# Kernel optimization log

Hardware: AMD Instinct MI355X
Metric: run time of the kernel (lower is better)

Reference implementation:

```python
import jax, jax.numpy as jnp
import numpy as np

N_HEAD = 16
D_K = 64
D_V = 64
D_MODEL = 1024
B = 2
S = 2048
LN_EPS = 1e-6
NEG = -1000000000.0


def setup_inputs() -> dict:
    key = jax.random.key(0)
    ks = jax.random.split(key, 6)
    scale = 1.0 / np.sqrt(D_MODEL)
    return {
        "qkv": jax.random.normal(ks[0], (B, S, D_MODEL), dtype=jnp.float32),
        "mask": jax.random.randint(ks[1], (B, S, S), 0, 2, dtype=jnp.int32),
        "w_qs": jax.random.normal(ks[2], (D_MODEL, N_HEAD * D_K), dtype=jnp.float32) * scale,
        "w_ks": jax.random.normal(ks[3], (D_MODEL, N_HEAD * D_K), dtype=jnp.float32) * scale,
        "w_vs": jax.random.normal(ks[4], (D_MODEL, N_HEAD * D_V), dtype=jnp.float32) * scale,
        "w_fc": jax.random.normal(ks[5], (N_HEAD * D_V, D_MODEL), dtype=jnp.float32) * scale,
        "ln_gamma": jnp.ones((D_MODEL,), dtype=jnp.float32),
        "ln_beta": jnp.zeros((D_MODEL,), dtype=jnp.float32),
    }


def reference(qkv, mask, w_qs, w_ks, w_vs, w_fc, ln_gamma, ln_beta):
    b, s, d = qkv.shape
    temperature = jnp.asarray(D_K, qkv.dtype) ** 0.5
    residual = qkv
    # projections -> [b, h, s, d_k/d_v]
    q = (qkv @ w_qs).reshape(b, s, N_HEAD, D_K).transpose(0, 2, 1, 3)
    k = (qkv @ w_ks).reshape(b, s, N_HEAD, D_K).transpose(0, 2, 1, 3)
    v = (qkv @ w_vs).reshape(b, s, N_HEAD, D_V).transpose(0, 2, 1, 3)
    # scaled dot-product attention with mask
    attn = jnp.einsum('bhqd,bhkd->bhqk', q / temperature, k)
    attn = jnp.where(mask[:, None, :, :] == 0, jnp.asarray(NEG, attn.dtype), attn)
    attn = jax.nn.softmax(attn, axis=-1)
    out = jnp.einsum('bhqk,bhkd->bhqd', attn, v)
    # merge heads, output projection, residual + layernorm
    out = out.transpose(0, 2, 1, 3).reshape(b, s, N_HEAD * D_V)
    out = out @ w_fc
    out = out + residual
    mu = jnp.mean(out, axis=-1, keepdims=True)
    var = jnp.var(out, axis=-1, keepdims=True)
    out = (out - mu) * jax.lax.rsqrt(var + LN_EPS) * ln_gamma + ln_beta
    return out, attn
```

## Files before the change

### kernel.cpp

```cpp
#include <hip/hip_runtime.h>
#include <stdint.h>

#define D_MODEL 1024
#define NHEAD   16
#define BATCH   2
#define SEQ     2048
#define MROWS   (BATCH*SEQ)
#define OUT0_ELEMS (MROWS*D_MODEL)
#define W_ELEMS    (D_MODEL*D_MODEL)

#define U_QKV_HI  0
#define U_QKV_LO  4194304
#define U_WQ_HI   8388608
#define U_WQ_LO   9437184
#define U_WK_HI   10485760
#define U_WK_LO   11534336
#define U_WV      12582912
#define U_WFC     13631488
#define F_Q       7340032
#define F_K       11534336
#define U_VT      31457280
#define B_MB      71303168
#define F_G       2097152

typedef __bf16  bf16x8 __attribute__((ext_vector_type(8)));
typedef float   f32x4  __attribute__((ext_vector_type(4)));

__device__ __forceinline__ float bf2f(unsigned short u) {
    union { unsigned int ui; float f; } v; v.ui = ((unsigned int)u) << 16; return v.f;
}
__device__ __forceinline__ unsigned short f2bf(float f) {
    union { float f; unsigned int u; } v; v.f = f;
    unsigned int u = v.u;
    return (unsigned short)((u + 0x7FFFu + ((u >> 16) & 1u)) >> 16);
}
__device__ __forceinline__ void split2(float x, unsigned short& hi, unsigned short& lo) {
    hi = f2bf(x);
    lo = f2bf(x - bf2f(hi));
}

__global__ void k_split(const float* in, unsigned short* hiA, unsigned short* loA)
{
    int i = (blockIdx.x * 256 + threadIdx.x) * 4;
    float4 x = *(const float4*)&in[i];
    ushort4 h, l;
    split2(x.x, h.x, l.x); split2(x.y, h.y, l.y);
    split2(x.z, h.z, l.z); split2(x.w, h.w, l.w);
    *(ushort4*)&hiA[i] = h;
    *(ushort4*)&loA[i] = l;
}

__global__ void k_wtrans(const float* w0, const float* w1, const float* w2,
                         const float* w3, unsigned short* R)
{
    __shared__ __align__(16) float T[64][68];
    int z = blockIdx.z;
    const float* in = (z == 0) ? w0 : (z == 1) ? w1 : (z == 2) ? w2 : w3;
    const int hiOff[4] = {U_WQ_HI, U_WK_HI, U_WV, U_WFC};
    const int loOff[2] = {U_WQ_LO, U_WK_LO};
    unsigned short* outH = R + hiOff[z];
    unsigned short* outL = (z < 2) ? (R + loOff[z]) : nullptr;
    int bn = blockIdx.x, bk = blockIdx.y, tid = threadIdx.x;
    int r0 = tid >> 4, c = (tid & 15) * 4;
    for (int i = 0; i < 4; i++) {
        int r = r0 + i * 16;
        *(float4*)&T[r][c] = *(const float4*)&in[(bk*64 + r)*1024 + bn*64 + c];
    }
    __syncthreads();
    for (int i = 0; i < 4; i++) {
        int r = r0 + i * 16;
        ushort4 h, l;
        split2(T[c+0][r], h.x, l.x); split2(T[c+1][r], h.y, l.y);
        split2(T[c+2][r], h.z, l.z); split2(T[c+3][r], h.w, l.w);
        *(ushort4*)&outH[(bn*64 + r)*1024 + bk*64 + c] = h;
        if (z < 2) *(ushort4*)&outL[(bn*64 + r)*1024 + bk*64 + c] = l;
    }
}

__global__ void k_maskpack(const int* mask, unsigned long long* mb)
{
    int w = blockIdx.x * 4 + (threadIdx.x >> 6);
    int lane = threadIdx.x & 63;
    int v = mask[(size_t)w * 64 + lane];
    unsigned long long bal = __ballot(v != 0);
    if (lane == 0) mb[w] = bal;
}

__global__ __launch_bounds__(256)
void k_gemm_qk(const unsigned short* R, float* ws_f)
{
    __shared__ __align__(16) unsigned short Ah[8192], Al[8192];
    __shared__ __align__(16) unsigned short Bh[8192], Bl[8192];
    int tid = threadIdx.x, wv = tid >> 6, lane = tid & 63;
    int quad = lane >> 4, l15 = lane & 15;
    int m0 = blockIdx.y * 128, n0 = blockIdx.x * 128;
    int z = blockIdx.z;
    const unsigned short* Ahg = R + U_QKV_HI;
    const unsigned short* Alg = R + U_QKV_LO;
    const unsigned short* Bhg = R + (z == 0 ? U_WQ_HI : U_WK_HI);
    const unsigned short* Blg = R + (z == 0 ? U_WQ_LO : U_WK_LO);
    float* out = ws_f + (z == 0 ? F_Q : F_K);
    float scale = (z == 0) ? 0.125f : 1.0f;

    f32x4 zero4 = {0.f, 0.f, 0.f, 0.f};
    f32x4 acc[4][4];
    for (int a = 0; a < 4; a++) for (int b = 0; b < 4; b++) acc[a][b] = zero4;
    int wr = (wv >> 1) * 64, wc = (wv & 1) * 64;

    for (int k0 = 0; k0 < 1024; k0 += 64) {
        __syncthreads();
        for (int i = 0; i < 4; i++) {
            int e = (tid + 256*i) * 8, row = e >> 6, col = e & 63;
            *(uint4*)&Ah[e] = *(const uint4*)&Ahg[(m0+row)*1024 + k0 + col];
            *(uint4*)&Al[e] = *(const uint4*)&Alg[(m0+row)*1024 + k0 + col];
            *(uint4*)&Bh[e] = *(const uint4*)&Bhg[(n0+row)*1024 + k0 + col];
            *(uint4*)&Bl[e] = *(const uint4*)&Blg[(n0+row)*1024 + k0 + col];
        }
        __syncthreads();
        #pragma unroll
        for (int kc = 0; kc < 2; kc++) {
            bf16x8 ah[4], al[4], bh[4], bl[4];
            #pragma unroll
            for (int t = 0; t < 4; t++) {
                int ao = (wr + t*16 + l15)*64 + kc*32 + quad*8;
                int bo = (wc + t*16 + l15)*64 + kc*32 + quad*8;
                ah[t] = *(const bf16x8*)&Ah[ao];
                al[t] = *(const bf16x8*)&Al[ao];
                bh[t] = *(const bf16x8*)&Bh[bo];
                bl[t] = *(const bf16x8*)&Bl[bo];
            }
            #pragma unroll
            for (int tm = 0; tm < 4; tm++)
                #pragma unroll
                for (int tn = 0; tn < 4; tn++) {
                    acc[tm][tn] = __builtin_amdgcn_mfma_f32_16x16x32_bf16(ah[tm], bh[tn], acc[tm][tn], 0,0,0);
                    acc[tm][tn] = __builtin_amdgcn_mfma_f32_16x16x32_bf16(ah[tm], bl[tn], acc[tm][tn], 0,0,0);
                    acc[tm][tn] = __builtin_amdgcn_mfma_f32_16x16x32_bf16(al[tm], bh[tn], acc[tm][tn], 0,0,0);
                }
        }
    }
    for (int tm = 0; tm < 4; tm++) for (int tn = 0; tn < 4; tn++)
        for (int r = 0; r < 4; r++) {
            int row = m0 + wr + tm*16 + quad*4 + r;
            int col = n0 + wc + tn*16 + l15;
            out[(size_t)row*1024 + col] = acc[tm][tn][r] * scale;
        }
}

__global__ __launch_bounds__(256)
void k_gemm_bf(const unsigned short* A, const unsigned short* Bt,
               unsigned short* Vt, float* Gf, const float* resf, int mode)
{
    __shared__ __align__(16) unsigned short As[8192];
    __shared__ __align__(16) unsigned short Bs[8192];
    int tid = threadIdx.x, wv = tid >> 6, lane = tid & 63;
    int quad = lane >> 4, l15 = lane & 15;
    int m0 = blockIdx.y * 128, n0 = blockIdx.x * 128;
    f32x4 zero4 = {0.f, 0.f, 0.f, 0.f};
    f32x4 acc[4][4];
    for (int a = 0; a < 4; a++) for (int b = 0; b < 4; b++) acc[a][b] = zero4;
    int wr = (wv >> 1) * 64, wc = (wv & 1) * 64;

    for (int k0 = 0; k0 < 1024; k0 += 64) {
        __syncthreads();
        for (int i = 0; i < 4; i++) {
            int e = (tid + 256*i) * 8, row = e >> 6, col = e & 63;
            *(uint4*)&As[e] = *(const uint4*)&A [(m0+row)*1024 + k0 + col];
            *(uint4*)&Bs[e] = *(const uint4*)&Bt[(n0+row)*1024 + k0 + col];
        }
        __syncthreads();
        #pragma unroll
        for (int kc = 0; kc < 2; kc++) {
            bf16x8 af[4], bfr[4];
            #pragma unroll
            for (int t = 0; t < 4; t++) {
                af[t]  = *(const bf16x8*)&As[(wr + t*16 + l15)*64 + kc*32 + quad*8];
                bfr[t] = *(const bf16x8*)&Bs[(wc + t*16 + l15)*64 + kc*32 + quad*8];
            }
            #pragma unroll
            for (int tm = 0; tm < 4; tm++)
                #pragma unroll
                for (int tn = 0; tn < 4; tn++)
                    acc[tm][tn] = __builtin_amdgcn_mfma_f32_16x16x32_bf16(
                        af[tm], bfr[tn], acc[tm][tn], 0, 0, 0);
        }
    }
    for (int tm = 0; tm < 4; tm++) for (int tn = 0; tn < 4; tn++)
        for (int r = 0; r < 4; r++) {
            int row = m0 + wr + tm*16 + quad*4 + r;
            int col = n0 + wc + tn*16 + l15;
            float v = acc[tm][tn][r];
            if (mode == 1) {
                Gf[(size_t)row*1024 + col] = v + resf[(size_t)row*1024 + col];
            } else {
                int b = row >> 11, s = row & 2047, h = col >> 6, d = col & 63;
                Vt[(size_t)(((b*16 + h)*64 + d))*2048 + s] = f2bf(v);
            }
        }
}

__global__ __launch_bounds__(256)
void k_attn(const float* Q, const float* K, const unsigned short* Vt,
            const unsigned long long* mb, float* Pout, unsigned short* Obuf)
{
    __shared__ __align__(16) unsigned short Qh[128*64], Ql[128*64];
    __shared__ __align__(16) unsigned short Kh[32*64],  Kl[32*64];
    __shared__ __align__(16) unsigned short Vs[64*32];
    __shared__ __align__(16) unsigned short Ps[128*32];
    int tid = threadIdx.x, wv = tid >> 6, lane = tid & 63;
    int quad = lane >> 4, l15 = lane & 15;
    int h = blockIdx.x, qt = blockIdx.y, b = blockIdx.z;

    const float* Qb = Q + (size_t)(b*2048 + qt*128)*1024 + h*64;
    const float* Kb = K + (size_t)b*2048*1024 + h*64;
    const unsigned short* Vtb = Vt + (size_t)((b*16 + h)*64)*2048;
    const unsigned long long* Mb = mb + (size_t)(b*2048 + qt*128)*32;
    float* Pg = Pout + (size_t)((b*16 + h)*2048 + qt*128)*2048;

    for (int i = 0; i < 8; i++) {
        int e = (tid + 256*i)*4, row = e >> 6, col = e & 63;
        float4 x = *(const float4*)&Qb[(size_t)row*1024 + col];
        ushort4 hv, lv;
        split2(x.x, hv.x, lv.x); split2(x.y, hv.y, lv.y);
        split2(x.z, hv.z, lv.z); split2(x.w, hv.w, lv.w);
        *(ushort4*)&Qh[row*64 + col] = hv;
        *(ushort4*)&Ql[row*64 + col] = lv;
    }

    float lsum[8];
    for (int r = 0; r < 8; r++) lsum[r] = 0.f;
    f32x4 zero4 = {0.f, 0.f, 0.f, 0.f};

    for (int kt = 0; kt < 64; kt++) {
        __syncthreads();
        for (int i = 0; i < 2; i++) {
            int e = (tid + 256*i)*4, row = e >> 6, col = e & 63;
            float4 x = *(const float4*)&Kb[(size_t)(kt*32 + row)*1024 + col];
            ushort4 hv, lv;
            split2(x.x, hv.x, lv.x); split2(x.y, hv.y, lv.y);
            split2(x.z, hv.z, lv.z); split2(x.w, hv.w, lv.w);
            *(ushort4*)&Kh[row*64 + col] = hv;
            *(ushort4*)&Kl[row*64 + col] = lv;
        }
        __syncthreads();
        f32x4 sacc[2][2];
        for (int a = 0; a < 2; a++) for (int c = 0; c < 2; c++) sacc[a][c] = zero4;
        #pragma unroll
        for (int kc = 0; kc < 2; kc++) {
            bf16x8 qh[2], ql[2], kh[2], kl[2];
            #pragma unroll
            for (int t = 0; t < 2; t++) {
                int qo = (wv*32 + t*16 + l15)*64 + kc*32 + quad*8;
                int ko = (t*16 + l15)*64 + kc*32 + quad*8;
                qh[t] = *(const bf16x8*)&Qh[qo]; ql[t] = *(const bf16x8*)&Ql[qo];
                kh[t] = *(const bf16x8*)&Kh[ko]; kl[t] = *(const bf16x8*)&Kl[ko];
            }
            #pragma unroll
            for (int tm = 0; tm < 2; tm++)
                #pragma unroll
                for (int tn = 0; tn < 2; tn++) {
                    sacc[tm][tn] = __builtin_amdgcn_mfma_f32_16x16x32_bf16(qh[tm], kh[tn], sacc[tm][tn], 0,0,0);
                    sacc[tm][tn] = __builtin_amdgcn_mfma_f32_16x16x32_bf16(qh[tm], kl[tn], sacc[tm][tn], 0,0,0);
                    sacc[tm][tn] = __builtin_amdgcn_mfma_f32_16x16x32_bf16(ql[tm], kh[tn], sacc[tm][tn], 0,0,0);
                }
        }
        #pragma unroll
        for (int tm = 0; tm < 2; tm++)
            #pragma unroll
            for (int r = 0; r < 4; r++) {
                int row = wv*32 + tm*16 + quad*4 + r;
                unsigned long long w = Mb[row*32 + (kt >> 1)];
                int base = (kt & 1) * 32;
                float acc = 0.f;
                #pragma unroll
                for (int tn = 0; tn < 2; tn++)
                    if ((w >> (base + tn*16 + l15)) & 1ull) acc += __expf(sacc[tm][tn][r]);
                lsum[tm*4 + r] += acc;
            }
    }
    float invl[8];
    for (int r = 0; r < 8; r++) {
        float v = lsum[r];
        v += __shfl_xor(v, 1); v += __shfl_xor(v, 2);
        v += __shfl_xor(v, 4); v += __shfl_xor(v, 8);
        invl[r] = 1.0f / fmaxf(v, 1e-30f);
    }

    f32x4 oacc[2][4];
    for (int a = 0; a < 2; a++) for (int c = 0; c < 4; c++) oacc[a][c] = zero4;

    for (int kt = 0; kt < 64; kt++) {
        __syncthreads();
        for (int i = 0; i < 2; i++) {
            int e = (tid + 256*i)*4, row = e >> 6, col = e & 63;
            float4 x = *(const float4*)&Kb[(size_t)(kt*32 + row)*1024 + col];
            ushort4 hv, lv;
            split2(x.x, hv.x, lv.x); split2(x.y, hv.y, lv.y);
            split2(x.z, hv.z, lv.z); split2(x.w, hv.w, lv.w);
            *(ushort4*)&Kh[row*64 + col] = hv;
            *(ushort4*)&Kl[row*64 + col] = lv;
        }
        {
            int d = tid >> 2, sl = (tid & 3) * 8;
            *(uint4*)&Vs[d*32 + sl] = *(const uint4*)&Vtb[(size_t)d*2048 + kt*32 + sl];
        }
        __syncthreads();
        f32x4 sacc[2][2];
        for (int a = 0; a < 2; a++) for (int c = 0; c < 2; c++) sacc[a][c] = zero4;
        #pragma unroll
        for (int kc = 0; kc < 2; kc++) {
            bf16x8 qh[2], ql[2], kh[2], kl[2];
            #pragma unroll
            for (int t = 0; t < 2; t++) {
                int qo = (wv*32 + t*16 + l15)*64 + kc*32 + quad*8;
                int ko = (t*16 + l15)*64 + kc*32 + quad*8;
                qh[t] = *(const bf16x8*)&Qh[qo]; ql[t] = *(const bf16x8*)&Ql[qo];
                kh[t] = *(const bf16x8*)&Kh[ko]; kl[t] = *(const bf16x8*)&Kl[ko];
            }
            #pragma unroll
            for (int tm = 0; tm < 2; tm++)
                #pragma unroll
                for (int tn = 0; tn < 2; tn++) {
                    sacc[tm][tn] = __builtin_amdgcn_mfma_f32_16x16x32_bf16(qh[tm], kh[tn], sacc[tm][tn], 0,0,0);
                    sacc[tm][tn] = __builtin_amdgcn_mfma_f32_16x16x32_bf16(qh[tm], kl[tn], sacc[tm][tn], 0,0,0);
                    sacc[tm][tn] = __builtin_amdgcn_mfma_f32_16x16x32_bf16(ql[tm], kh[tn], sacc[tm][tn], 0,0,0);
                }
        }
        #pragma unroll
        for (int tm = 0; tm < 2; tm++)
            #pragma unroll
            for (int r = 0; r < 4; r++) {
                int row = wv*32 + tm*16 + quad*4 + r;
                unsigned long long w = Mb[row*32 + (kt >> 1)];
                int base = (kt & 1) * 32;
                float il = invl[tm*4 + r];
                #pragma unroll
                for (int tn = 0; tn < 2; tn++) {
                    float p = ((w >> (base + tn*16 + l15)) & 1ull)
                              ? __expf(sacc[tm][tn][r]) * il : 0.0f;
                    Ps[row*32 + tn*16 + l15] = f2bf(p);
                    Pg[(size_t)row*2048 + kt*32 + tn*16 + l15] = p;
                }
            }
        __syncthreads();
        {
            bf16x8 ap[2], bv[4];
            #pragma unroll
            for (int t = 0; t < 2; t++)
                ap[t] = *(const bf16x8*)&Ps[(wv*32 + t*16 + l15)*32 + quad*8];
            #pragma unroll
            for (int t = 0; t < 4; t++)
                bv[t] = *(const bf16x8*)&Vs[(t*16 + l15)*32 + quad*8];
            #pragma unroll
            for (int tm = 0; tm < 2; tm++)
                #pragma unroll
                for (int nd = 0; nd < 4; nd++)
                    oacc[tm][nd] = __builtin_amdgcn_mfma_f32_16x16x32_bf16(
                        ap[tm], bv[nd], oacc[tm][nd], 0, 0, 0);
        }
    }
    for (int tm = 0; tm < 2; tm++) for (int nd = 0; nd < 4; nd++)
        for (int r = 0; r < 4; r++) {
            int row = wv*32 + tm*16 + quad*4 + r;
            int grow = b*2048 + qt*128 + row;
            Obuf[(size_t)grow*1024 + h*64 + nd*16 + l15] = f2bf(oacc[tm][nd][r]);
        }
}

__global__ void k_ln(const float* G, const float* gamma, const float* beta,
                     float* out)
{
    int r = blockIdx.x, tid = threadIdx.x;
    float4 x = *(const float4*)&G[(size_t)r*1024 + tid*4];
    float s  = x.x + x.y + x.z + x.w;
    float sq = x.x*x.x + x.y*x.y + x.z*x.z + x.w*x.w;
    for (int d = 1; d < 64; d <<= 1) { s += __shfl_xor(s, d); sq += __shfl_xor(sq, d); }
    __shared__ float ssum[4], ssq[4];
    int wv = tid >> 6, lane = tid & 63;
    if (lane == 0) { ssum[wv] = s; ssq[wv] = sq; }
    __syncthreads();
    float ts = ssum[0] + ssum[1] + ssum[2] + ssum[3];
    float tq = ssq[0] + ssq[1] + ssq[2] + ssq[3];
    float mu  = ts * (1.0f/1024.0f);
    float var = tq * (1.0f/1024.0f) - mu*mu;
    float rs  = rsqrtf(var + 1e-6f);
    float4 o;
    int c = tid*4;
    o.x = (x.x - mu) * rs * gamma[c+0] + beta[c+0];
    o.y = (x.y - mu) * rs * gamma[c+1] + beta[c+1];
    o.z = (x.z - mu) * rs * gamma[c+2] + beta[c+2];
    o.w = (x.w - mu) * rs * gamma[c+3] + beta[c+3];
    *(float4*)&out[(size_t)r*1024 + c] = o;
}

extern "C" void kernel_launch(void* const* d_in, const int* in_sizes, int n_in,
                              void* d_out, int out_size, void* d_ws, size_t ws_size,
                              hipStream_t stream)
{
    const float* qkv   = (const float*)d_in[0];
    const int*   mask  = (const int*)d_in[1];
    const float* wq    = (const float*)d_in[2];
    const float* wk    = (const float*)d_in[3];
    const float* wvp   = (const float*)d_in[4];
    const float* wfc   = (const float*)d_in[5];
    const float* gamma = (const float*)d_in[6];
    const float* beta  = (const float*)d_in[7];

    unsigned short* R   = (unsigned short*)d_ws;
    float*          Wf  = (float*)d_ws;
    unsigned short* Vtb = R + U_VT;
    unsigned short* Ob  = R + U_QKV_HI;
    float*          Gf  = Wf + F_G;
    unsigned long long* MB = (unsigned long long*)((char*)d_ws + B_MB);

    float* outp  = (float*)d_out;
    float* attnp = outp + OUT0_ELEMS;

    k_split   <<<4096, 256, 0, stream>>>(qkv, R + U_QKV_HI, R + U_QKV_LO);
    k_wtrans  <<<dim3(16,16,4), 256, 0, stream>>>(wq, wk, wvp, wfc, R);
    k_maskpack<<<32768, 256, 0, stream>>>(mask, MB);
    k_gemm_qk <<<dim3(8,32,2), 256, 0, stream>>>(R, Wf);
    k_gemm_bf <<<dim3(8,32,1), 256, 0, stream>>>(R + U_QKV_HI, R + U_WV,
                                                 Vtb, nullptr, nullptr, 0);
    k_attn    <<<dim3(16,16,2), 256, 0, stream>>>(Wf + F_Q, Wf + F_K, Vtb, MB,
                                                  attnp, Ob);
    k_gemm_bf <<<dim3(8,32,1), 256, 0, stream>>>(Ob, R + U_WFC,
                                                 nullptr, Gf, qkv, 1);
    k_ln      <<<4096, 256, 0, stream>>>(Gf, gamma, beta, outp);
}
```

Measured before the change: 1.074 ms.

## Pre-split Q/K to bf16 hi/lo head-major, use LDS direct loads, widen attention key tiles

The Q/K projection GEMM now writes bf16 hi/lo splits in a head-major [b,h,s,d] layout instead of fp32. The attention kernel can then load Q, K and V tiles with global_load_lds directly, with no per-tile fp32 split. Key tiles grow from 32 to 64 columns, which halves loop iterations and removes one barrier per PV step, and the P staging buffer gets a padded stride. The GEMM kernels also switch to direct-to-LDS loads. The workspace layout is reshuffled, and reusing the old weight region for V^T relies on stage ordering being correct.

```diff
diff --git a/kernel.cpp b/kernel.cpp
--- a/kernel.cpp
+++ b/kernel.cpp
@@ -9,19 +9,22 @@
 #define OUT0_ELEMS (MROWS*D_MODEL)
 #define W_ELEMS    (D_MODEL*D_MODEL)
 
-#define U_QKV_HI  0
-#define U_QKV_LO  4194304
-#define U_WQ_HI   8388608
-#define U_WQ_LO   9437184
-#define U_WK_HI   10485760
-#define U_WK_LO   11534336
-#define U_WV      12582912
-#define U_WFC     13631488
-#define F_Q       7340032
-#define F_K       11534336
-#define U_VT      31457280
-#define B_MB      71303168
-#define F_G       2097152
+#define U_QKVH 0
+#define U_QKVL 4194304
+#define U_WQH  8388608
+#define U_WQL  9437184
+#define U_WKH  10485760
+#define U_WKL  11534336
+#define U_WV   12582912
+#define U_WFC  13631488
+#define U_QH   14680064
+#define U_QL   18874368
+#define U_KH   23068672
+#define U_KL   27262976
+#define U_VT   8388608
+#define U_MB   31457280
+#define F_G    2097152
+#define PS_LD  80
 
 typedef __bf16  bf16x8 __attribute__((ext_vector_type(8)));
 typedef float   f32x4  __attribute__((ext_vector_type(4)));
@@ -37,6 +40,11 @@
 __device__ __forceinline__ void split2(float x, unsigned short& hi, unsigned short& lo) {
     hi = f2bf(x);
     lo = f2bf(x - bf2f(hi));
+}
+__device__ __forceinline__ void gld16(const void* g, void* l) {
+    __builtin_amdgcn_global_load_lds(
+        (const __attribute__((address_space(1))) unsigned int*)g,
+        (__attribute__((address_space(3))) unsigned int*)l, 16, 0, 0);
 }
 
 __global__ void k_split(const float* in, unsigned short* hiA, unsigned short* loA)
@@ -56,8 +64,8 @@
     __shared__ __align__(16) float T[64][68];
     int z = blockIdx.z;
     const float* in = (z == 0) ? w0 : (z == 1) ? w1 : (z == 2) ? w2 : w3;
-    const int hiOff[4] = {U_WQ_HI, U_WK_HI, U_WV, U_WFC};
-    const int loOff[2] = {U_WQ_LO, U_WK_LO};
+    const int hiOff[4] = {U_WQH, U_WKH, U_WV, U_WFC};
+    const int loOff[2] = {U_WQL, U_WKL};
     unsigned short* outH = R + hiOff[z];
     unsigned short* outL = (z < 2) ? (R + loOff[z]) : nullptr;
     int bn = blockIdx.x, bk = blockIdx.y, tid = threadIdx.x;
@@ -87,7 +95,7 @@
 }
 
 __global__ __launch_bounds__(256)
-void k_gemm_qk(const unsigned short* R, float* ws_f)
+void k_gemm_qk(const unsigned short* R, unsigned short* RW)
 {
     __shared__ __align__(16) unsigned short Ah[8192], Al[8192];
     __shared__ __align__(16) unsigned short Bh[8192], Bl[8192];
@@ -95,11 +103,12 @@
     int quad = lane >> 4, l15 = lane & 15;
     int m0 = blockIdx.y * 128, n0 = blockIdx.x * 128;
     int z = blockIdx.z;
-    const unsigned short* Ahg = R + U_QKV_HI;
-    const unsigned short* Alg = R + U_QKV_LO;
-    const unsigned short* Bhg = R + (z == 0 ? U_WQ_HI : U_WK_HI);
-    const unsigned short* Blg = R + (z == 0 ? U_WQ_LO : U_WK_LO);
-    float* out = ws_f + (z == 0 ? F_Q : F_K);
+    const unsigned short* Ahg = R + U_QKVH;
+    const unsigned short* Alg = R + U_QKVL;
+    const unsigned short* Bhg = R + (z == 0 ? U_WQH : U_WKH);
+    const unsigned short* Blg = R + (z == 0 ? U_WQL : U_WKL);
+    unsigned short* outH = RW + (z == 0 ? U_QH : U_KH);
+    unsigned short* outL = RW + (z == 0 ? U_QL : U_KL);
     float scale = (z == 0) ? 0.125f : 1.0f;
 
     f32x4 zero4 = {0.f, 0.f, 0.f, 0.f};
@@ -111,10 +120,10 @@
         __syncthreads();
         for (int i = 0; i < 4; i++) {
             int e = (tid + 256*i) * 8, row = e >> 6, col = e & 63;
-            *(uint4*)&Ah[e] = *(const uint4*)&Ahg[(m0+row)*1024 + k0 + col];
-            *(uint4*)&Al[e] = *(const uint4*)&Alg[(m0+row)*1024 + k0 + col];
-            *(uint4*)&Bh[e] = *(const uint4*)&Bhg[(n0+row)*1024 + k0 + col];
-            *(uint4*)&Bl[e] = *(const uint4*)&Blg[(n0+row)*1024 + k0 + col];
+            gld16(&Ahg[(m0+row)*1024 + k0 + col], &Ah[e]);
+            gld16(&Alg[(m0+row)*1024 + k0 + col], &Al[e]);
+            gld16(&Bhg[(n0+row)*1024 + k0 + col], &Bh[e]);
+            gld16(&Blg[(n0+row)*1024 + k0 + col], &Bl[e]);
         }
         __syncthreads();
         #pragma unroll
@@ -143,7 +152,12 @@
         for (int r = 0; r < 4; r++) {
             int row = m0 + wr + tm*16 + quad*4 + r;
             int col = n0 + wc + tn*16 + l15;
-            out[(size_t)row*1024 + col] = acc[tm][tn][r] * scale;
+            int bb = row >> 11, s = row & 2047, hh = col >> 6, d = col & 63;
+            size_t idx = ((size_t)(bb*16 + hh)*2048 + s)*64 + d;
+            unsigned short hv, lv;
+            split2(acc[tm][tn][r] * scale, hv, lv);
+            outH[idx] = hv;
+            outL[idx] = lv;
         }
 }
 
@@ -165,8 +179,8 @@
         __syncthreads();
         for (int i = 0; i < 4; i++) {
             int e = (tid + 256*i) * 8, row = e >> 6, col = e & 63;
-            *(uint4*)&As[e] = *(const uint4*)&A [(m0+row)*1024 + k0 + col];
-            *(uint4*)&Bs[e] = *(const uint4*)&Bt[(n0+row)*1024 + k0 + col];
+            gld16(&A [(m0+row)*1024 + k0 + col], &As[e]);
+            gld16(&Bt[(n0+row)*1024 + k0 + col], &Bs[e]);
         }
         __syncthreads();
         #pragma unroll
@@ -200,65 +214,63 @@
 }
 
 __global__ __launch_bounds__(256)
-void k_attn(const float* Q, const float* K, const unsigned short* Vt,
-            const unsigned long long* mb, float* Pout, unsigned short* Obuf)
+void k_attn(const unsigned short* R, const unsigned long long* mb,
+            float* Pout, unsigned short* Obuf)
 {
     __shared__ __align__(16) unsigned short Qh[128*64], Ql[128*64];
-    __shared__ __align__(16) unsigned short Kh[32*64],  Kl[32*64];
-    __shared__ __align__(16) unsigned short Vs[64*32];
-    __shared__ __align__(16) unsigned short Ps[128*32];
+    __shared__ __align__(16) unsigned short Kh[64*64],  Kl[64*64];
+    __shared__ __align__(16) unsigned short Vs[64*64];
+    __shared__ __align__(16) unsigned short Ps[128*PS_LD];
     int tid = threadIdx.x, wv = tid >> 6, lane = tid & 63;
     int quad = lane >> 4, l15 = lane & 15;
     int h = blockIdx.x, qt = blockIdx.y, b = blockIdx.z;
-
-    const float* Qb = Q + (size_t)(b*2048 + qt*128)*1024 + h*64;
-    const float* Kb = K + (size_t)b*2048*1024 + h*64;
-    const unsigned short* Vtb = Vt + (size_t)((b*16 + h)*64)*2048;
+    int bh = b*16 + h;
+
+    const unsigned short* Qhg = R + U_QH + ((size_t)bh*2048 + qt*128)*64;
+    const unsigned short* Qlg = R + U_QL + ((size_t)bh*2048 + qt*128)*64;
+    const unsigned short* Khg = R + U_KH + (size_t)bh*2048*64;
+    const unsigned short* Klg = R + U_KL + (size_t)bh*2048*64;
+    const unsigned short* Vtg = R + U_VT + (size_t)bh*64*2048;
     const unsigned long long* Mb = mb + (size_t)(b*2048 + qt*128)*32;
-    float* Pg = Pout + (size_t)((b*16 + h)*2048 + qt*128)*2048;
-
-    for (int i = 0; i < 8; i++) {
-        int e = (tid + 256*i)*4, row = e >> 6, col = e & 63;
-        float4 x = *(const float4*)&Qb[(size_t)row*1024 + col];
-        ushort4 hv, lv;
-        split2(x.x, hv.x, lv.x); split2(x.y, hv.y, lv.y);
-        split2(x.z, hv.z, lv.z); split2(x.w, hv.w, lv.w);
-        *(ushort4*)&Qh[row*64 + col] = hv;
-        *(ushort4*)&Ql[row*64 + col] = lv;
+    float* Pg = Pout + ((size_t)bh*2048 + qt*128)*2048;
+
+    for (int i = 0; i < 4; i++) {
+        int e = (tid + 256*i)*8;
+        gld16(&Qhg[e], &Qh[e]);
+        gld16(&Qlg[e], &Ql[e]);
     }
 
     float lsum[8];
     for (int r = 0; r < 8; r++) lsum[r] = 0.f;
     f32x4 zero4 = {0.f, 0.f, 0.f, 0.f};
 
-    for (int kt = 0; kt < 64; kt++) {
+    for (int kt = 0; kt < 32; kt++) {
         __syncthreads();
         for (int i = 0; i < 2; i++) {
-            int e = (tid + 256*i)*4, row = e >> 6, col = e & 63;
-            float4 x = *(const float4*)&Kb[(size_t)(kt*32 + row)*1024 + col];
-            ushort4 hv, lv;
-            split2(x.x, hv.x, lv.x); split2(x.y, hv.y, lv.y);
-            split2(x.z, hv.z, lv.z); split2(x.w, hv.w, lv.w);
-            *(ushort4*)&Kh[row*64 + col] = hv;
-            *(ushort4*)&Kl[row*64 + col] = lv;
-        }
-        __syncthreads();
-        f32x4 sacc[2][2];
-        for (int a = 0; a < 2; a++) for (int c = 0; c < 2; c++) sacc[a][c] = zero4;
+            int e = (tid + 256*i)*8;
+            gld16(&Khg[kt*4096 + e], &Kh[e]);
+            gld16(&Klg[kt*4096 + e], &Kl[e]);
+        }
+        __syncthreads();
+        f32x4 sacc[2][4];
+        for (int a = 0; a < 2; a++) for (int c = 0; c < 4; c++) sacc[a][c] = zero4;
         #pragma unroll
         for (int kc = 0; kc < 2; kc++) {
-            bf16x8 qh[2], ql[2], kh[2], kl[2];
+            bf16x8 qh[2], ql[2], kh[4], kl[4];
             #pragma unroll
             for (int t = 0; t < 2; t++) {
                 int qo = (wv*32 + t*16 + l15)*64 + kc*32 + quad*8;
+                qh[t] = *(const bf16x8*)&Qh[qo]; ql[t] = *(const bf16x8*)&Ql[qo];
+            }
+            #pragma unroll
+            for (int t = 0; t < 4; t++) {
                 int ko = (t*16 + l15)*64 + kc*32 + quad*8;
-                qh[t] = *(const bf16x8*)&Qh[qo]; ql[t] = *(const bf16x8*)&Ql[qo];
                 kh[t] = *(const bf16x8*)&Kh[ko]; kl[t] = *(const bf16x8*)&Kl[ko];
             }
             #pragma unroll
             for (int tm = 0; tm < 2; tm++)
                 #pragma unroll
-                for (int tn = 0; tn < 2; tn++) {
+                for (int tn = 0; tn < 4; tn++) {
                     sacc[tm][tn] = __builtin_amdgcn_mfma_f32_16x16x32_bf16(qh[tm], kh[tn], sacc[tm][tn], 0,0,0);
                     sacc[tm][tn] = __builtin_amdgcn_mfma_f32_16x16x32_bf16(qh[tm], kl[tn], sacc[tm][tn], 0,0,0);
                     sacc[tm][tn] = __builtin_amdgcn_mfma_f32_16x16x32_bf16(ql[tm], kh[tn], sacc[tm][tn], 0,0,0);
@@ -269,12 +281,11 @@
             #pragma unroll
             for (int r = 0; r < 4; r++) {
                 int row = wv*32 + tm*16 + quad*4 + r;
-                unsigned long long w = Mb[row*32 + (kt >> 1)];
-                int base = (kt & 1) * 32;
+                unsigned long long w = Mb[row*32 + kt];
                 float acc = 0.f;
                 #pragma unroll
-                for (int tn = 0; tn < 2; tn++)
-                    if ((w >> (base + tn*16 + l15)) & 1ull) acc += __expf(sacc[tm][tn][r]);
+                for (int tn = 0; tn < 4; tn++)
+                    if ((w >> (tn*16 + l15)) & 1ull) acc += __expf(sacc[tm][tn][r]);
                 lsum[tm*4 + r] += acc;
             }
     }
@@ -289,38 +300,34 @@
     f32x4 oacc[2][4];
     for (int a = 0; a < 2; a++) for (int c = 0; c < 4; c++) oacc[a][c] = zero4;
 
-    for (int kt = 0; kt < 64; kt++) {
+    for (int kt = 0; kt < 32; kt++) {
         __syncthreads();
         for (int i = 0; i < 2; i++) {
-            int e = (tid + 256*i)*4, row = e >> 6, col = e & 63;
-            float4 x = *(const float4*)&Kb[(size_t)(kt*32 + row)*1024 + col];
-            ushort4 hv, lv;
-            split2(x.x, hv.x, lv.x); split2(x.y, hv.y, lv.y);
-            split2(x.z, hv.z, lv.z); split2(x.w, hv.w, lv.w);
-            *(ushort4*)&Kh[row*64 + col] = hv;
-            *(ushort4*)&Kl[row*64 + col] = lv;
-        }
-        {
-            int d = tid >> 2, sl = (tid & 3) * 8;
-            *(uint4*)&Vs[d*32 + sl] = *(const uint4*)&Vtb[(size_t)d*2048 + kt*32 + sl];
-        }
-        __syncthreads();
-        f32x4 sacc[2][2];
-        for (int a = 0; a < 2; a++) for (int c = 0; c < 2; c++) sacc[a][c] = zero4;
+            int e = (tid + 256*i)*8, d = e >> 6, s = e & 63;
+            gld16(&Khg[kt*4096 + e], &Kh[e]);
+            gld16(&Klg[kt*4096 + e], &Kl[e]);
+            gld16(&Vtg[(size_t)d*2048 + kt*64 + s], &Vs[e]);
+        }
+        __syncthreads();
+        f32x4 sacc[2][4];
+        for (int a = 0; a < 2; a++) for (int c = 0; c < 4; c++) sacc[a][c] = zero4;
         #pragma unroll
         for (int kc = 0; kc < 2; kc++) {
-            bf16x8 qh[2], ql[2], kh[2], kl[2];
+            bf16x8 qh[2], ql[2], kh[4], kl[4];
             #pragma unroll
             for (int t = 0; t < 2; t++) {
                 int qo = (wv*32 + t*16 + l15)*64 + kc*32 + quad*8;
+                qh[t] = *(const bf16x8*)&Qh[qo]; ql[t] = *(const bf16x8*)&Ql[qo];
+            }
+            #pragma unroll
+            for (int t = 0; t < 4; t++) {
                 int ko = (t*16 + l15)*64 + kc*32 + quad*8;
-                qh[t] = *(const bf16x8*)&Qh[qo]; ql[t] = *(const bf16x8*)&Ql[qo];
                 kh[t] = *(const bf16x8*)&Kh[ko]; kl[t] = *(const bf16x8*)&Kl[ko];
             }
             #pragma unroll
             for (int tm = 0; tm < 2; tm++)
                 #pragma unroll
-                for (int tn = 0; tn < 2; tn++) {
+                for (int tn = 0; tn < 4; tn++) {
                     sacc[tm][tn] = __builtin_amdgcn_mfma_f32_16x16x32_bf16(qh[tm], kh[tn], sacc[tm][tn], 0,0,0);
                     sacc[tm][tn] = __builtin_amdgcn_mfma_f32_16x16x32_bf16(qh[tm], kl[tn], sacc[tm][tn], 0,0,0);
                     sacc[tm][tn] = __builtin_amdgcn_mfma_f32_16x16x32_bf16(ql[tm], kh[tn], sacc[tm][tn], 0,0,0);
@@ -331,26 +338,25 @@
             #pragma unroll
             for (int r = 0; r < 4; r++) {
                 int row = wv*32 + tm*16 + quad*4 + r;
-                unsigned long long w = Mb[row*32 + (kt >> 1)];
-                int base = (kt & 1) * 32;
+                unsigned long long w = Mb[row*32 + kt];
                 float il = invl[tm*4 + r];
                 #pragma unroll
-                for (int tn = 0; tn < 2; tn++) {
-                    float p = ((w >> (base + tn*16 + l15)) & 1ull)
+                for (int tn = 0; tn < 4; tn++) {
+                    float p = ((w >> (tn*16 + l15)) & 1ull)
                               ? __expf(sacc[tm][tn][r]) * il : 0.0f;
-                    Ps[row*32 + tn*16 + l15] = f2bf(p);
-                    Pg[(size_t)row*2048 + kt*32 + tn*16 + l15] = p;
+                    Ps[row*PS_LD + tn*16 + l15] = f2bf(p);
+                    Pg[(size_t)row*2048 + kt*64 + tn*16 + l15] = p;
                 }
             }
-        __syncthreads();
-        {
+        #pragma unroll
+        for (int kc = 0; kc < 2; kc++) {
             bf16x8 ap[2], bv[4];
             #pragma unroll
             for (int t = 0; t < 2; t++)
-                ap[t] = *(const bf16x8*)&Ps[(wv*32 + t*16 + l15)*32 + quad*8];
+                ap[t] = *(const bf16x8*)&Ps[(wv*32 + t*16 + l15)*PS_LD + kc*32 + quad*8];
             #pragma unroll
             for (int t = 0; t < 4; t++)
-                bv[t] = *(const bf16x8*)&Vs[(t*16 + l15)*32 + quad*8];
+                bv[t] = *(const bf16x8*)&Vs[(t*16 + l15)*64 + kc*32 + quad*8];
             #pragma unroll
             for (int tm = 0; tm < 2; tm++)
                 #pragma unroll
@@ -408,22 +414,20 @@
 
     unsigned short* R   = (unsigned short*)d_ws;
     float*          Wf  = (float*)d_ws;
-    unsigned short* Vtb = R + U_VT;
-    unsigned short* Ob  = R + U_QKV_HI;
+    unsigned short* Ob  = R + U_QKVH;
     float*          Gf  = Wf + F_G;
-    unsigned long long* MB = (unsigned long long*)((char*)d_ws + B_MB);
+    unsigned long long* MB = (unsigned long long*)(R + U_MB);
 
     float* outp  = (float*)d_out;
     float* attnp = outp + OUT0_ELEMS;
 
-    k_split   <<<4096, 256, 0, stream>>>(qkv, R + U_QKV_HI, R + U_QKV_LO);
+    k_split   <<<4096, 256, 0, stream>>>(qkv, R + U_QKVH, R + U_QKVL);
     k_wtrans  <<<dim3(16,16,4), 256, 0, stream>>>(wq, wk, wvp, wfc, R);
     k_maskpack<<<32768, 256, 0, stream>>>(mask, MB);
-    k_gemm_qk <<<dim3(8,32,2), 256, 0, stream>>>(R, Wf);
-    k_gemm_bf <<<dim3(8,32,1), 256, 0, stream>>>(R + U_QKV_HI, R + U_WV,
-                                                 Vtb, nullptr, nullptr, 0);
-    k_attn    <<<dim3(16,16,2), 256, 0, stream>>>(Wf + F_Q, Wf + F_K, Vtb, MB,
-                                                  attnp, Ob);
+    k_gemm_qk <<<dim3(8,32,2), 256, 0, stream>>>(R, R);
+    k_gemm_bf <<<dim3(8,32,1), 256, 0, stream>>>(R + U_QKVH, R + U_WV,
+                                                 R + U_VT, nullptr, nullptr, 0);
+    k_attn    <<<dim3(16,16,2), 256, 0, stream>>>(R, MB, attnp, Ob);
     k_gemm_bf <<<dim3(8,32,1), 256, 0, stream>>>(Ob, R + U_WFC,
                                                  nullptr, Gf, qkv, 1);
     k_ln      <<<4096, 256, 0, stream>>>(Gf, gamma, beta, outp);
```

After: 923.0 us. -14.0%, faster.
